# Optimization experiments

Hardware: AMD Instinct MI355X
Metric: run time of the kernel (lower is better)

Reference implementation:

```python
import jax, jax.numpy as jnp
import numpy as np

H = 4096        # hidden_size
I = 11008       # intermediate_size
R = 32          # low-rank error-correction rank
NLEV = 16       # int4 -> 16 levels
Q_ZERO = 7.5    # symmetric int4 zero point
Q_STEP = 0.005  # per-channel scale multiplier (keeps dequantized weights ~N(0, 1/sqrt(H)) scale)
LR_SCALE = 0.02 # low-rank correction magnitude


def setup_inputs() -> dict:
    key = jax.random.key(0)
    ks = jax.random.split(key, 13)
    B, S = 2, 2048
    inp = {
        "x": jax.random.normal(ks[0], (B, S, H), jnp.float32),
        "gate_q": jax.random.randint(ks[1], (I, H), 0, NLEV, jnp.int32),
        "gate_scale": jax.random.uniform(ks[2], (I,), jnp.float32),
        "gate_A": jax.random.normal(ks[3], (H, R), jnp.float32),
        "gate_B": jax.random.normal(ks[4], (R, I), jnp.float32),
        "up_q": jax.random.randint(ks[5], (I, H), 0, NLEV, jnp.int32),
        "up_scale": jax.random.uniform(ks[6], (I,), jnp.float32),
        "up_A": jax.random.normal(ks[7], (H, R), jnp.float32),
        "up_B": jax.random.normal(ks[8], (R, I), jnp.float32),
        "down_q": jax.random.randint(ks[9], (H, I), 0, NLEV, jnp.int32),
        "down_scale": jax.random.uniform(ks[10], (H,), jnp.float32),
        "down_A": jax.random.normal(ks[11], (I, R), jnp.float32),
        "down_B": jax.random.normal(ks[12], (R, H), jnp.float32),
    }
    return inp


def _qlinear(x, q, scale, A, Bm):
    # Dequantize int4 weight [out, in] with per-output-channel scale, then
    # y = x @ W^T + LR_SCALE * (x @ A) @ B   (LQER low-rank error correction)
    w = (q.astype(jnp.float32) - Q_ZERO) * (scale * Q_STEP)[:, None]
    y = jnp.einsum('bsh,oh->bso', x, w)
    return y + LR_SCALE * ((x @ A) @ Bm)


def reference(x, gate_q, gate_scale, gate_A, gate_B,
              up_q, up_scale, up_A, up_B,
              down_q, down_scale, down_A, down_B):
    g = _qlinear(x, gate_q, gate_scale, gate_A, gate_B)   # [B,S,I]
    u = _qlinear(x, up_q, up_scale, up_A, up_B)           # [B,S,I]
    h = jax.nn.silu(g) * u                                # SwiGLU gating
    return _qlinear(h, down_q, down_scale, down_A, down_B)  # [B,S,H]
```

## Files before the change

kernel.cpp:

```cpp
#include <hip/hip_runtime.h>
#include <hip/hip_bf16.h>
#include <stdint.h>

#define H_DIM 4096
#define I_DIM 11008
#define M_TOK 4096

typedef __attribute__((ext_vector_type(8))) short short8;
typedef __attribute__((ext_vector_type(4))) float f32x4;
typedef __attribute__((ext_vector_type(4))) int   i32x4;

#define SX_DIV 6.0f
#define QS  (0.0025f * SX_DIV / 127.0f)
#define SH_MAX 768.0f
#define QSD (0.0025f * SH_MAX / 127.0f)

static __device__ __forceinline__ float bf2f(unsigned short u) {
    union { uint32_t i; float f; } v; v.i = ((uint32_t)u) << 16; return v.f;
}
static __device__ __forceinline__ unsigned short f2bf(float f) {
    union { float f; uint32_t i; } v; v.f = f;
    uint32_t r = v.i + 0x7FFF + ((v.i >> 16) & 1);
    return (unsigned short)(r >> 16);
}

static __device__ __forceinline__ void gload16(const void* g, void* l) {
    __builtin_amdgcn_global_load_lds(
        (const __attribute__((address_space(1))) void*)g,
        (__attribute__((address_space(3))) void*)l, 16, 0, 0);
}

__global__ void k_prep_all(
    const float* __restrict__ x,
    const int* __restrict__ gq, const int* __restrict__ uq,
    const int* __restrict__ dq,
    const float* __restrict__ gA, const float* __restrict__ uA,
    const float* __restrict__ dA,
    const float* __restrict__ gB, const float* __restrict__ uB,
    const float* __restrict__ dB,
    unsigned short* __restrict__ xbf, char* __restrict__ xi8,
    char* __restrict__ Wg8, char* __restrict__ Wu8, char* __restrict__ Wd8,
    unsigned short* __restrict__ AgT, unsigned short* __restrict__ AuT,
    unsigned short* __restrict__ AdT,
    unsigned short* __restrict__ BgT, unsigned short* __restrict__ BuT,
    unsigned short* __restrict__ BdT)
{
    const int stride = gridDim.x * blockDim.x;
    const int tid0 = blockIdx.x * blockDim.x + threadIdx.x;
    const int XN4 = (M_TOK * H_DIM) / 4;
    const float SXI = 127.0f / SX_DIV;
    for (int i = tid0; i < XN4; i += stride) {
        f32x4 v = ((const f32x4*)x)[i];
        uint64_t p = (uint64_t)f2bf(v[0]) | ((uint64_t)f2bf(v[1]) << 16) |
                     ((uint64_t)f2bf(v[2]) << 32) | ((uint64_t)f2bf(v[3]) << 48);
        ((uint64_t*)xbf)[i] = p;
        uint32_t q8 = 0;
#pragma unroll
        for (int t = 0; t < 4; t++) {
            int a = (int)lrintf(v[t] * SXI);
            a = a > 127 ? 127 : (a < -127 ? -127 : a);
            q8 |= ((uint32_t)(a & 255)) << (8 * t);
        }
        ((uint32_t*)xi8)[i] = q8;
    }
    const int QN4 = (I_DIM * H_DIM) / 4;
    for (int i = tid0; i < 3 * QN4; i += stride) {
        int j = i; const int* src; char* dst;
        if (j < QN4) { src = gq; dst = Wg8; }
        else if ((j -= QN4) < QN4) { src = uq; dst = Wu8; }
        else { j -= QN4; src = dq; dst = Wd8; }
        i32x4 qv = ((const i32x4*)src)[j];
        uint32_t p = 0;
#pragma unroll
        for (int t = 0; t < 4; t++)
            p |= ((uint32_t)((2 * qv[t] - 15) & 255)) << (8 * t);
        ((uint32_t*)dst)[j] = p;
    }
    const int AT = 32 * H_DIM;
    for (int i = tid0; i < 2 * AT; i += stride) {
        int j = i; const float* src; unsigned short* dst;
        if (j < AT) { src = gA; dst = AgT; } else { j -= AT; src = uA; dst = AuT; }
        int r = j >> 12, k = j & 4095;
        dst[j] = f2bf(src[k * 32 + r]);
    }
    const int ATD = 32 * I_DIM;
    for (int i = tid0; i < ATD; i += stride) {
        int r = i / I_DIM, k = i - r * I_DIM;
        AdT[i] = f2bf(dA[k * 32 + r]);
    }
    const int TBI = I_DIM * 32, TBH = H_DIM * 32;
    for (int i = tid0; i < 2 * TBI + TBH; i += stride) {
        int j = i; const float* src; unsigned short* dst; int N;
        if (j < TBI) { src = gB; dst = BgT; N = I_DIM; }
        else if ((j -= TBI) < TBI) { src = uB; dst = BuT; N = I_DIM; }
        else { j -= TBI; src = dB; dst = BdT; N = H_DIM; }
        int n = j >> 5, r = j & 31;
        dst[j] = f2bf(src[r * N + n]);
    }
}

__global__ __launch_bounds__(256) void k_T(
    const unsigned short* __restrict__ in,
    const unsigned short* __restrict__ AT,
    unsigned short* __restrict__ T,
    int K)
{
    const int wid = threadIdx.x >> 6, lane = threadIdx.x & 63;
    const int base = blockIdx.x * 64 + wid * 16;
    const int l15 = lane & 15, kg = (lane >> 4) * 8;
    f32x4 acc0 = {}, acc1 = {};
    for (int k0 = 0; k0 < K; k0 += 32) {
        short8 af = *(const short8*)&in[(size_t)(base + l15) * K + k0 + kg];
        short8 b0 = *(const short8*)&AT[(size_t)l15 * K + k0 + kg];
        short8 b1 = *(const short8*)&AT[(size_t)(16 + l15) * K + k0 + kg];
        acc0 = __builtin_amdgcn_mfma_f32_16x16x32_bf16(af, b0, acc0, 0, 0, 0);
        acc1 = __builtin_amdgcn_mfma_f32_16x16x32_bf16(af, b1, acc1, 0, 0, 0);
    }
    const int q4 = lane >> 4;
#pragma unroll
    for (int t = 0; t < 4; t++) {
        int m = base + q4 * 4 + t;
        T[m * 32 + l15]      = f2bf(acc0[t] * 0.02f);
        T[m * 32 + 16 + l15] = f2bf(acc1[t] * 0.02f);
    }
}

__global__ __launch_bounds__(512, 1) void k_gemmfu8(
    const char* __restrict__ Xq,
    const char* __restrict__ Wg8,
    const char* __restrict__ Wu8,
    const unsigned short* __restrict__ Tg,
    const unsigned short* __restrict__ Tu,
    const unsigned short* __restrict__ BgT,
    const unsigned short* __restrict__ BuT,
    const float* __restrict__ gs, const float* __restrict__ us,
    unsigned short* __restrict__ H,
    char* __restrict__ Hq,
    int M, int NI, int K)
{
    extern __shared__ char dynsmem[];
    char* smem = dynsmem;
    const int tid = threadIdx.x, wid = tid >> 6, lane = tid & 63;
    const int wr = wid >> 2, wc = wid & 3;

    const int gx = NI >> 7;
    const int nwg = gx * (M >> 8);
    int orig = blockIdx.y * gx + blockIdx.x;
    int q8 = nwg >> 3, r8 = nwg & 7;
    int xcd = orig & 7, lid = orig >> 3;
    int wg = (xcd < r8 ? xcd * (q8 + 1) : r8 * (q8 + 1) + (xcd - r8) * q8) + lid;
    const int bcol = (wg % gx) << 7;
    const int brow = (wg / gx) << 8;

    const int srow = wid * 16 + (lane >> 2);
    const int scolB = ((lane & 3) ^ ((lane >> 3) & 3)) * 16;
    const char* aSrc  = Xq  + (size_t)(brow + srow) * K + scolB;
    const char* bgSrc = Wg8 + (size_t)(bcol + srow) * K + scolB;
    const char* buSrc = Wu8 + (size_t)(bcol + srow) * K + scolB;
    const int ldwB = wid * 1024;

    i32x4 acc[8][4];
#pragma unroll
    for (int i = 0; i < 8; ++i)
#pragma unroll
        for (int j = 0; j < 4; ++j) acc[i][j] = (i32x4){0, 0, 0, 0};

    i32x4 A0f[4], A1f[4], BgAf[2], BgBf[2], Buf[2];
    const int l15 = lane & 15, q4b = lane >> 4;
    const int ps = (q4b ^ ((l15 >> 1) & 3)) * 16;
    const char* aRd = smem + (wr * 64 + l15) * 64 + ps;
    const char* bRd = smem + 16384 + (wc * 32 + l15) * 64 + ps;
    const int NT = K >> 6;

#define SA0(BB, k0) gload16(aSrc + (k0), smem + (BB)*32768 + ldwB)
#define SA1(BB, k0) gload16(aSrc + 128*(size_t)K + (k0), smem + (BB)*32768 + 8192 + ldwB)
#define SBG(BB, k0) gload16(bgSrc + (k0), smem + (BB)*32768 + 16384 + ldwB)
#define SBU(BB, k0) gload16(buSrc + (k0), smem + (BB)*32768 + 24576 + ldwB)
#define LDA0(BB) { _Pragma("unroll") for (int i4 = 0; i4 < 4; ++i4) \
    A0f[i4] = *(const i32x4*)(aRd + (BB)*32768 + i4*1024); }
#define LDA1(BB) { _Pragma("unroll") for (int i4 = 0; i4 < 4; ++i4) \
    A1f[i4] = *(const i32x4*)(aRd + (BB)*32768 + 8192 + i4*1024); }
#define LDBG(SET, BB) { _Pragma("unroll") for (int j2 = 0; j2 < 2; ++j2) \
    SET[j2] = *(const i32x4*)(bRd + (BB)*32768 + j2*1024); }
#define LDBU(BB) { _Pragma("unroll") for (int j2 = 0; j2 < 2; ++j2) \
    Buf[j2] = *(const i32x4*)(bRd + (BB)*32768 + 8192 + j2*1024); }
#define MFI(AF, BF, IH, JB) { __builtin_amdgcn_s_setprio(1); \
    _Pragma("unroll") for (int i4 = 0; i4 < 4; ++i4) \
    _Pragma("unroll") for (int j2 = 0; j2 < 2; ++j2) \
        acc[(IH)*4+i4][(JB)*2+j2] = __builtin_amdgcn_mfma_i32_16x16x64_i8( \
            AF[i4], BF[j2], acc[(IH)*4+i4][(JB)*2+j2], 0, 0, 0); \
    __builtin_amdgcn_s_setprio(0); }
#define BARR() __builtin_amdgcn_s_barrier()

#define FTILE(BB, BGC, BGN, k2, S2, CERT, RN) { \
    LDBU(BB); \
    BARR(); \
    MFI(A0f, BGC, 0, 0); \
    LDA1(BB); \
    BARR(); \
    if (S2) { SA0(BB, k2); SBG(BB, k2); } \
    MFI(A0f, Buf, 0, 1); \
    if (CERT == 1) asm volatile("s_waitcnt vmcnt(2)" ::: "memory"); \
    if (CERT == 2) asm volatile("s_waitcnt vmcnt(0)" ::: "memory"); \
    BARR(); \
    if (S2) { SBU(BB, k2); } \
    MFI(A1f, Buf, 1, 1); \
    if (RN) { LDA0(1-(BB)); LDBG(BGN, 1-(BB)); } \
    BARR(); \
    if (S2) { SA1(BB, k2); } \
    MFI(A1f, BGC, 1, 0); \
}

    SA0(0, 0); SBG(0, 0); SBU(0, 0); SA1(0, 0);
    SA0(1, 64); SBG(1, 64); SBU(1, 64); SA1(1, 64);
    asm volatile("s_waitcnt vmcnt(4)" ::: "memory");
    BARR();
    LDA0(0); LDBG(BgAf, 0);

    for (int u = 0; u < (NT - 2) / 2; ++u) {
        const int k2a = (2 * u + 2) << 6, k2b = (2 * u + 3) << 6;
        FTILE(0, BgAf, BgBf, k2a, 1, 1, 1);
        FTILE(1, BgBf, BgAf, k2b, 1, 1, 1);
    }
    FTILE(0, BgAf, BgBf, 0, 0, 2, 1);
    FTILE(1, BgBf, BgAf, 0, 0, 0, 0);

#undef FTILE
#undef BARR
#undef MFI
#undef LDBU
#undef LDBG
#undef LDA1
#undef LDA0
#undef SBU
#undef SBG
#undef SA1
#undef SA0

    __builtin_amdgcn_s_barrier();
    {
        const int scolH = (lane & 3) * 8;
        gload16(Tg + (size_t)(brow + srow) * 32 + scolH,        smem + ldwB);
        gload16(Tg + (size_t)(brow + 128 + srow) * 32 + scolH,  smem + 8192 + ldwB);
        gload16(Tu + (size_t)(brow + srow) * 32 + scolH,        smem + 16384 + ldwB);
        gload16(Tu + (size_t)(brow + 128 + srow) * 32 + scolH,  smem + 24576 + ldwB);
        gload16(BgT + (size_t)(bcol + srow) * 32 + scolH,       smem + 32768 + ldwB);
        gload16(BuT + (size_t)(bcol + srow) * 32 + scolH,       smem + 40960 + ldwB);
    }
    asm volatile("s_waitcnt vmcnt(0)" ::: "memory");
    __builtin_amdgcn_s_barrier();

    const int fr = l15;
    short8 BgF[2], BuF[2];
#pragma unroll
    for (int j2 = 0; j2 < 2; ++j2) {
        BgF[j2] = *(const short8*)(smem + 32768 + (wc * 32 + j2 * 16 + l15) * 64 + q4b * 16);
        BuF[j2] = *(const short8*)(smem + 40960 + (wc * 32 + j2 * 16 + l15) * 64 + q4b * 16);
    }
    float cg[2], cu[2];
#pragma unroll
    for (int j2 = 0; j2 < 2; ++j2) {
        int n = bcol + wc * 32 + j2 * 16 + fr;
        cg[j2] = gs[n] * QS;
        cu[j2] = us[n] * QS;
    }
    const int q4 = lane >> 4;
    const float HSI = 127.0f / SH_MAX;
#pragma unroll
    for (int i = 0; i < 8; ++i) {
        int trow = (i >> 2) * 128 + wr * 64 + (i & 3) * 16 + l15;
        short8 tgf = *(const short8*)(smem + trow * 64 + q4b * 16);
        short8 tuf = *(const short8*)(smem + 16384 + trow * 64 + q4b * 16);
#pragma unroll
        for (int j2 = 0; j2 < 2; ++j2) {
            f32x4 ag, au;
#pragma unroll
            for (int t = 0; t < 4; ++t) {
                ag[t] = (float)acc[i][j2][t] * cg[j2];
                au[t] = (float)acc[i][2 + j2][t] * cu[j2];
            }
            ag = __builtin_amdgcn_mfma_f32_16x16x32_bf16(tgf, BgF[j2], ag, 0, 0, 0);
            au = __builtin_amdgcn_mfma_f32_16x16x32_bf16(tuf, BuF[j2], au, 0, 0, 0);
#pragma unroll
            for (int t = 0; t < 4; ++t) {
                int m = brow + (i >> 2) * 128 + wr * 64 + (i & 3) * 16 + q4 * 4 + t;
                int n = bcol + wc * 32 + j2 * 16 + fr;
                float g = ag[t];
                float s = g / (1.0f + __expf(-g));
                float h = s * au[t];
                H[(size_t)m * NI + n] = f2bf(h);
                int a = (int)lrintf(h * HSI);
                a = a > 127 ? 127 : (a < -127 ? -127 : a);
                Hq[(size_t)m * NI + n] = (char)a;
            }
        }
    }
}

__global__ __launch_bounds__(512, 1) void k_gemmd8(
    const char* __restrict__ Hq,
    const char* __restrict__ Wd8,
    const unsigned short* __restrict__ Td,
    const unsigned short* __restrict__ BdT,
    const float* __restrict__ ds,
    float* __restrict__ C,
    int M, int N, int K)
{
    extern __shared__ char dynsmem[];
    char* smem = dynsmem;
    const int tid = threadIdx.x, wid = tid >> 6, lane = tid & 63;
    const int wr = wid >> 2, wc = wid & 3;

    const int gx = N >> 8;
    const int nwg = gx * (M >> 8);
    int orig = blockIdx.y * gx + blockIdx.x;
    int q8 = nwg >> 3, r8 = nwg & 7;
    int xcd = orig & 7, lid = orig >> 3;
    int wg = (xcd < r8 ? xcd * (q8 + 1) : r8 * (q8 + 1) + (xcd - r8) * q8) + lid;
    const int bcol = (wg % gx) << 8;
    const int brow = (wg / gx) << 8;

    const int srow = wid * 16 + (lane >> 2);
    const int scolB = ((lane & 3) ^ ((lane >> 3) & 3)) * 16;
    const char* aSrc  = Hq  + (size_t)(brow + srow) * K + scolB;
    const char* bgSrc = Wd8 + (size_t)(bcol + srow) * K + scolB;
    const char* buSrc = Wd8 + (size_t)(bcol + 128 + srow) * K + scolB;
    const int ldwB = wid * 1024;

    i32x4 acc[8][4];
#pragma unroll
    for (int i = 0; i < 8; ++i)
#pragma unroll
        for (int j = 0; j < 4; ++j) acc[i][j] = (i32x4){0, 0, 0, 0};

    i32x4 A0f[4], A1f[4], BgAf[2], BgBf[2], Buf[2];
    const int l15 = lane & 15, q4b = lane >> 4;
    const int ps = (q4b ^ ((l15 >> 1) & 3)) * 16;
    const char* aRd = smem + (wr * 64 + l15) * 64 + ps;
    const char* bRd = smem + 16384 + (wc * 32 + l15) * 64 + ps;
    const int NT = K >> 6;

#define SA0(BB, k0) gload16(aSrc + (k0), smem + (BB)*32768 + ldwB)
#define SA1(BB, k0) gload16(aSrc + 128*(size_t)K + (k0), smem + (BB)*32768 + 8192 + ldwB)
#define SBG(BB, k0) gload16(bgSrc + (k0), smem + (BB)*32768 + 16384 + ldwB)
#define SBU(BB, k0) gload16(buSrc + (k0), smem + (BB)*32768 + 24576 + ldwB)
#define LDA0(BB) { _Pragma("unroll") for (int i4 = 0; i4 < 4; ++i4) \
    A0f[i4] = *(const i32x4*)(aRd + (BB)*32768 + i4*1024); }
#define LDA1(BB) { _Pragma("unroll") for (int i4 = 0; i4 < 4; ++i4) \
    A1f[i4] = *(const i32x4*)(aRd + (BB)*32768 + 8192 + i4*1024); }
#define LDBG(SET, BB) { _Pragma("unroll") for (int j2 = 0; j2 < 2; ++j2) \
    SET[j2] = *(const i32x4*)(bRd + (BB)*32768 + j2*1024); }
#define LDBU(BB) { _Pragma("unroll") for (int j2 = 0; j2 < 2; ++j2) \
    Buf[j2] = *(const i32x4*)(bRd + (BB)*32768 + 8192 + j2*1024); }
#define MFI(AF, BF, IH, JB) { __builtin_amdgcn_s_setprio(1); \
    _Pragma("unroll") for (int i4 = 0; i4 < 4; ++i4) \
    _Pragma("unroll") for (int j2 = 0; j2 < 2; ++j2) \
        acc[(IH)*4+i4][(JB)*2+j2] = __builtin_amdgcn_mfma_i32_16x16x64_i8( \
            AF[i4], BF[j2], acc[(IH)*4+i4][(JB)*2+j2], 0, 0, 0); \
    __builtin_amdgcn_s_setprio(0); }
#define BARR() __builtin_amdgcn_s_barrier()

#define FTILE(BB, BGC, BGN, k2, S2, CERT, RN) { \
    LDBU(BB); \
    BARR(); \
    MFI(A0f, BGC, 0, 0); \
    LDA1(BB); \
    BARR(); \
    if (S2) { SA0(BB, k2); SBG(BB, k2); } \
    MFI(A0f, Buf, 0, 1); \
    if (CERT == 1) asm volatile("s_waitcnt vmcnt(2)" ::: "memory"); \
    if (CERT == 2) asm volatile("s_waitcnt vmcnt(0)" ::: "memory"); \
    BARR(); \
    if (S2) { SBU(BB, k2); } \
    MFI(A1f, Buf, 1, 1); \
    if (RN) { LDA0(1-(BB)); LDBG(BGN, 1-(BB)); } \
    BARR(); \
    if (S2) { SA1(BB, k2); } \
    MFI(A1f, BGC, 1, 0); \
}

    SA0(0, 0); SBG(0, 0); SBU(0, 0); SA1(0, 0);
    SA0(1, 64); SBG(1, 64); SBU(1, 64); SA1(1, 64);
    asm volatile("s_waitcnt vmcnt(4)" ::: "memory");
    BARR();
    LDA0(0); LDBG(BgAf, 0);

    for (int u = 0; u < (NT - 2) / 2; ++u) {
        const int k2a = (2 * u + 2) << 6, k2b = (2 * u + 3) << 6;
        FTILE(0, BgAf, BgBf, k2a, 1, 1, 1);
        FTILE(1, BgBf, BgAf, k2b, 1, 1, 1);
    }
    FTILE(0, BgAf, BgBf, 0, 0, 2, 1);
    FTILE(1, BgBf, BgAf, 0, 0, 0, 0);

#undef FTILE
#undef BARR
#undef MFI
#undef LDBU
#undef LDBG
#undef LDA1
#undef LDA0
#undef SBU
#undef SBG
#undef SA1
#undef SA0

    __builtin_amdgcn_s_barrier();
    {
        const int scolH = (lane & 3) * 8;
        gload16(Td + (size_t)(brow + srow) * 32 + scolH,         smem + ldwB);
        gload16(Td + (size_t)(brow + 128 + srow) * 32 + scolH,   smem + 8192 + ldwB);
        gload16(BdT + (size_t)(bcol + srow) * 32 + scolH,        smem + 16384 + ldwB);
        gload16(BdT + (size_t)(bcol + 128 + srow) * 32 + scolH,  smem + 24576 + ldwB);
    }
    asm volatile("s_waitcnt vmcnt(0)" ::: "memory");
    __builtin_amdgcn_s_barrier();

    const int fr = l15;
    short8 Bd0[2], Bd1[2];
#pragma unroll
    for (int j2 = 0; j2 < 2; ++j2) {
        Bd0[j2] = *(const short8*)(smem + 16384 + (wc * 32 + j2 * 16 + l15) * 64 + q4b * 16);
        Bd1[j2] = *(const short8*)(smem + 24576 + (wc * 32 + j2 * 16 + l15) * 64 + q4b * 16);
    }
    float c0[2], c1[2];
#pragma unroll
    for (int j2 = 0; j2 < 2; ++j2) {
        int n0 = bcol + wc * 32 + j2 * 16 + fr;
        c0[j2] = ds[n0] * QSD;
        c1[j2] = ds[n0 + 128] * QSD;
    }
    const int q4 = lane >> 4;
#pragma unroll
    for (int i = 0; i < 8; ++i) {
        int trow = (i >> 2) * 128 + wr * 64 + (i & 3) * 16 + l15;
        short8 tdf = *(const short8*)(smem + trow * 64 + q4b * 16);
#pragma unroll
        for (int j2 = 0; j2 < 2; ++j2) {
            f32x4 a0, a1;
#pragma unroll
            for (int t = 0; t < 4; ++t) {
                a0[t] = (float)acc[i][j2][t] * c0[j2];
                a1[t] = (float)acc[i][2 + j2][t] * c1[j2];
            }
            a0 = __builtin_amdgcn_mfma_f32_16x16x32_bf16(tdf, Bd0[j2], a0, 0, 0, 0);
            a1 = __builtin_amdgcn_mfma_f32_16x16x32_bf16(tdf, Bd1[j2], a1, 0, 0, 0);
#pragma unroll
            for (int t = 0; t < 4; ++t) {
                int m = brow + (i >> 2) * 128 + wr * 64 + (i & 3) * 16 + q4 * 4 + t;
                int n = bcol + wc * 32 + j2 * 16 + fr;
                C[(size_t)m * N + n] = a0[t];
                C[(size_t)m * N + n + 128] = a1[t];
            }
        }
    }
}

extern "C" void kernel_launch(void* const* d_in, const int* in_sizes, int n_in,
                              void* d_out, int out_size, void* d_ws, size_t ws_size,
                              hipStream_t stream) {
    (void)in_sizes; (void)n_in; (void)out_size; (void)ws_size;
    const float* x          = (const float*)d_in[0];
    const int*   gate_q     = (const int*)d_in[1];
    const float* gate_scale = (const float*)d_in[2];
    const float* gate_A     = (const float*)d_in[3];
    const float* gate_B     = (const float*)d_in[4];
    const int*   up_q       = (const int*)d_in[5];
    const float* up_scale   = (const float*)d_in[6];
    const float* up_A       = (const float*)d_in[7];
    const float* up_B       = (const float*)d_in[8];
    const int*   down_q     = (const int*)d_in[9];
    const float* down_scale = (const float*)d_in[10];
    const float* down_A     = (const float*)d_in[11];
    const float* down_B     = (const float*)d_in[12];

    char* ws = (char*)d_ws;
    size_t off = 0;
    auto alloc = [&](size_t bytes) {
        void* p = ws + off; off += (bytes + 255) & ~(size_t)255; return p;
    };
    unsigned short* xbf  = (unsigned short*)alloc((size_t)M_TOK * H_DIM * 2);
    char*           xi8  = (char*)alloc((size_t)M_TOK * H_DIM);
    char*           Wg8  = (char*)alloc((size_t)I_DIM * H_DIM);
    char*           Wu8  = (char*)alloc((size_t)I_DIM * H_DIM);
    char*           Wd8  = (char*)alloc((size_t)H_DIM * I_DIM);
    unsigned short* hbuf = (unsigned short*)alloc((size_t)M_TOK * I_DIM * 2);
    char*           hq   = (char*)alloc((size_t)M_TOK * I_DIM);
    unsigned short* Tg   = (unsigned short*)alloc((size_t)M_TOK * 32 * 2);
    unsigned short* Tu   = (unsigned short*)alloc((size_t)M_TOK * 32 * 2);
    unsigned short* Td   = (unsigned short*)alloc((size_t)M_TOK * 32 * 2);
    unsigned short* AgT  = (unsigned short*)alloc((size_t)32 * H_DIM * 2);
    unsigned short* AuT  = (unsigned short*)alloc((size_t)32 * H_DIM * 2);
    unsigned short* AdT  = (unsigned short*)alloc((size_t)32 * I_DIM * 2);
    unsigned short* BgT  = (unsigned short*)alloc((size_t)I_DIM * 32 * 2);
    unsigned short* BuT  = (unsigned short*)alloc((size_t)I_DIM * 32 * 2);
    unsigned short* BdT  = (unsigned short*)alloc((size_t)H_DIM * 32 * 2);

    (void)hipFuncSetAttribute((const void*)k_gemmfu8,
        hipFuncAttributeMaxDynamicSharedMemorySize, 65536);
    (void)hipFuncSetAttribute((const void*)k_gemmd8,
        hipFuncAttributeMaxDynamicSharedMemorySize, 65536);

    k_prep_all<<<2048, 256, 0, stream>>>(x, gate_q, up_q, down_q,
                                         gate_A, up_A, down_A,
                                         gate_B, up_B, down_B,
                                         xbf, xi8, Wg8, Wu8, Wd8, AgT, AuT, AdT,
                                         BgT, BuT, BdT);

    k_T<<<M_TOK / 64, 256, 0, stream>>>(xbf, AgT, Tg, H_DIM);
    k_T<<<M_TOK / 64, 256, 0, stream>>>(xbf, AuT, Tu, H_DIM);

    k_gemmfu8<<<dim3(I_DIM / 128, M_TOK / 256), 512, 65536, stream>>>(
        xi8, Wg8, Wu8, Tg, Tu, BgT, BuT, gate_scale, up_scale,
        hbuf, hq, M_TOK, I_DIM, H_DIM);

    k_T<<<M_TOK / 64, 256, 0, stream>>>(hbuf, AdT, Td, I_DIM);

    k_gemmd8<<<dim3(H_DIM / 256, M_TOK / 256), 512, 65536, stream>>>(
        hq, Wd8, Td, BdT, down_scale, (float*)d_out, M_TOK, H_DIM, I_DIM);
}
```

Before: 969.1 us.

## Split-K the low-rank projection kernels and fuse gate/up projections into one launch

Replaces the low-rank x@A projection kernel with split-K versions. Each block handles 16 rows, its 8 waves each take a slice of K, and partial sums are reduced through shared memory. The gate and up projections now share one launch that loads the x tile once. The aim is to raise the grid from 64 to 256 blocks and shorten each wave's serial K loop, since the old kernel badly underfilled the GPU. The cost is the shared-memory reduction and an extra barrier per block.

Result: faster. 776.4 us (-19.9%).

```diff
diff --git a/kernel.cpp b/kernel.cpp
--- a/kernel.cpp
+++ b/kernel.cpp
@@ -99,29 +99,90 @@
     }
 }
 
-__global__ __launch_bounds__(256) void k_T(
+__global__ __launch_bounds__(512) void k_Tdual(
+    const unsigned short* __restrict__ xbf,
+    const unsigned short* __restrict__ AgT,
+    const unsigned short* __restrict__ AuT,
+    unsigned short* __restrict__ Tg,
+    unsigned short* __restrict__ Tu)
+{
+    __shared__ float red[8 * 1024];
+    const int wid = threadIdx.x >> 6, lane = threadIdx.x & 63;
+    const int base = blockIdx.x * 16;
+    const int l15 = lane & 15, kg = (lane >> 4) * 8;
+    const int KC = H_DIM / 8;
+    const int k0w = wid * KC;
+    f32x4 g0 = {}, g1 = {}, u0 = {}, u1 = {};
+    for (int k0 = k0w; k0 < k0w + KC; k0 += 32) {
+        short8 af  = *(const short8*)&xbf[(size_t)(base + l15) * H_DIM + k0 + kg];
+        short8 bg0 = *(const short8*)&AgT[(size_t)l15 * H_DIM + k0 + kg];
+        short8 bg1 = *(const short8*)&AgT[(size_t)(16 + l15) * H_DIM + k0 + kg];
+        short8 bu0 = *(const short8*)&AuT[(size_t)l15 * H_DIM + k0 + kg];
+        short8 bu1 = *(const short8*)&AuT[(size_t)(16 + l15) * H_DIM + k0 + kg];
+        g0 = __builtin_amdgcn_mfma_f32_16x16x32_bf16(af, bg0, g0, 0, 0, 0);
+        g1 = __builtin_amdgcn_mfma_f32_16x16x32_bf16(af, bg1, g1, 0, 0, 0);
+        u0 = __builtin_amdgcn_mfma_f32_16x16x32_bf16(af, bu0, u0, 0, 0, 0);
+        u1 = __builtin_amdgcn_mfma_f32_16x16x32_bf16(af, bu1, u1, 0, 0, 0);
+    }
+    const int q4 = lane >> 4;
+    float* rw = red + wid * 1024;
+#pragma unroll
+    for (int t = 0; t < 4; t++) {
+        int row = q4 * 4 + t;
+        rw[row * 64 + l15]      = g0[t];
+        rw[row * 64 + 16 + l15] = g1[t];
+        rw[row * 64 + 32 + l15] = u0[t];
+        rw[row * 64 + 48 + l15] = u1[t];
+    }
+    __syncthreads();
+#pragma unroll
+    for (int e = threadIdx.x; e < 1024; e += 512) {
+        float s = 0.0f;
+#pragma unroll
+        for (int w = 0; w < 8; w++) s += red[w * 1024 + e];
+        int row = e >> 6, c = e & 63;
+        int m = base + row;
+        if (c < 32) Tg[m * 32 + c] = f2bf(s * 0.02f);
+        else        Tu[m * 32 + (c - 32)] = f2bf(s * 0.02f);
+    }
+}
+
+__global__ __launch_bounds__(512) void k_Tone(
     const unsigned short* __restrict__ in,
     const unsigned short* __restrict__ AT,
     unsigned short* __restrict__ T,
     int K)
 {
+    __shared__ float red[8 * 512];
     const int wid = threadIdx.x >> 6, lane = threadIdx.x & 63;
-    const int base = blockIdx.x * 64 + wid * 16;
+    const int base = blockIdx.x * 16;
     const int l15 = lane & 15, kg = (lane >> 4) * 8;
-    f32x4 acc0 = {}, acc1 = {};
-    for (int k0 = 0; k0 < K; k0 += 32) {
+    const int KC = K / 8;
+    const int k0w = wid * KC;
+    f32x4 a0 = {}, a1 = {};
+    for (int k0 = k0w; k0 < k0w + KC; k0 += 32) {
         short8 af = *(const short8*)&in[(size_t)(base + l15) * K + k0 + kg];
         short8 b0 = *(const short8*)&AT[(size_t)l15 * K + k0 + kg];
         short8 b1 = *(const short8*)&AT[(size_t)(16 + l15) * K + k0 + kg];
-        acc0 = __builtin_amdgcn_mfma_f32_16x16x32_bf16(af, b0, acc0, 0, 0, 0);
-        acc1 = __builtin_amdgcn_mfma_f32_16x16x32_bf16(af, b1, acc1, 0, 0, 0);
+        a0 = __builtin_amdgcn_mfma_f32_16x16x32_bf16(af, b0, a0, 0, 0, 0);
+        a1 = __builtin_amdgcn_mfma_f32_16x16x32_bf16(af, b1, a1, 0, 0, 0);
     }
     const int q4 = lane >> 4;
+    float* rw = red + wid * 512;
 #pragma unroll
     for (int t = 0; t < 4; t++) {
-        int m = base + q4 * 4 + t;
-        T[m * 32 + l15]      = f2bf(acc0[t] * 0.02f);
-        T[m * 32 + 16 + l15] = f2bf(acc1[t] * 0.02f);
+        int row = q4 * 4 + t;
+        rw[row * 32 + l15]      = a0[t];
+        rw[row * 32 + 16 + l15] = a1[t];
+    }
+    __syncthreads();
+    if (threadIdx.x < 512) {
+        int e = threadIdx.x;
+        float s = 0.0f;
+#pragma unroll
+        for (int w = 0; w < 8; w++) s += red[w * 512 + e];
+        int row = e >> 5, c = e & 31;
+        T[(base + row) * 32 + c] = f2bf(s * 0.02f);
     }
 }
 
@@ -507,14 +568,13 @@
                                          xbf, xi8, Wg8, Wu8, Wd8, AgT, AuT, AdT,
                                          BgT, BuT, BdT);
 
-    k_T<<<M_TOK / 64, 256, 0, stream>>>(xbf, AgT, Tg, H_DIM);
-    k_T<<<M_TOK / 64, 256, 0, stream>>>(xbf, AuT, Tu, H_DIM);
+    k_Tdual<<<M_TOK / 16, 512, 0, stream>>>(xbf, AgT, AuT, Tg, Tu);
 
     k_gemmfu8<<<dim3(I_DIM / 128, M_TOK / 256), 512, 65536, stream>>>(
         xi8, Wg8, Wu8, Tg, Tu, BgT, BuT, gate_scale, up_scale,
         hbuf, hq, M_TOK, I_DIM, H_DIM);
 
-    k_T<<<M_TOK / 64, 256, 0, stream>>>(hbuf, AdT, Td, I_DIM);
+    k_Tone<<<M_TOK / 16, 512, 0, stream>>>(hbuf, AdT, Td, I_DIM);
 
     k_gemmd8<<<dim3(H_DIM / 256, M_TOK / 256), 512, 65536, stream>>>(
         hq, Wd8, Td, BdT, down_scale, (float*)d_out, M_TOK, H_DIM, I_DIM);
```
